# Optimization experiments

Measured on AMD Instinct MI355X. Metric: run time of the kernel, lower is better.

The kernel has to match this reference:

```python
import jax, jax.numpy as jnp
import numpy as np

NEG_SLOPE = 0.2  # PyG GATConv default negative_slope


def gat_layer(x, src, dst, W, a_src, a_dst, bias, concat, N):
    """PyG GATConv: h = xW; e_ij = LeakyReLU(a_src.h_j + a_dst.h_i);
    alpha = segment-softmax over incoming edges of i; out_i = sum_j alpha_ij h_j."""
    H, C = a_src.shape
    h = (x @ W).reshape(N, H, C)                      # [N,H,C]
    alpha_s = jnp.einsum('nhc,hc->nh', h, a_src)      # [N,H]
    alpha_d = jnp.einsum('nhc,hc->nh', h, a_dst)      # [N,H]
    e = jax.nn.leaky_relu(alpha_s[src] + alpha_d[dst], NEG_SLOPE)  # [E,H]
    # numerically-stable segment softmax over destination nodes
    m = jax.ops.segment_max(e, dst, num_segments=N)   # [N,H]
    e = jnp.exp(e - m[dst])
    denom = jax.ops.segment_sum(e, dst, num_segments=N)
    alpha = e / (denom[dst] + 1e-16)                  # [E,H]
    msg = h[src] * alpha[:, :, None]                  # [E,H,C]
    out = jax.ops.segment_sum(msg, dst, num_segments=N)  # [N,H,C]
    out = out.reshape(N, H * C) if concat else out.mean(axis=1)
    return out + bias


def setup_inputs() -> dict:
    key = jax.random.key(0)
    ks = jax.random.split(key, 12)
    N, E, F_IN, C, H = 50000, 800000, 512, 32, 8
    s = 0.05
    x = jax.random.normal(ks[0], (N, F_IN), dtype=jnp.float32)
    edge_index = jax.random.randint(ks[1], (2, E), 0, N, dtype=jnp.int64)
    W1 = jax.random.normal(ks[2], (F_IN, H * C), dtype=jnp.float32) * s
    as1 = jax.random.normal(ks[3], (H, C), dtype=jnp.float32) * s
    ad1 = jax.random.normal(ks[4], (H, C), dtype=jnp.float32) * s
    b1 = jnp.zeros((H * C,), dtype=jnp.float32)
    W2 = jax.random.normal(ks[5], (H * C, H * C), dtype=jnp.float32) * s
    as2 = jax.random.normal(ks[6], (H, C), dtype=jnp.float32) * s
    ad2 = jax.random.normal(ks[7], (H, C), dtype=jnp.float32) * s
    b2 = jnp.zeros((C,), dtype=jnp.float32)
    Wp = jax.random.normal(ks[8], (C, 1), dtype=jnp.float32) * s
    bp = jnp.zeros((1,), dtype=jnp.float32)
    return {"edge_index": edge_index, "x": x, "W1": W1, "as1": as1, "ad1": ad1,
            "b1": b1, "W2": W2, "as2": as2, "ad2": ad2, "b2": b2,
            "Wp": Wp, "bp": bp}


def reference(edge_index, x, W1, as1, ad1, b1, W2, as2, ad2, b2, Wp, bp):
    N = x.shape[0]
    # PyG GATConv adds self-loops by default
    loops = jnp.arange(N, dtype=edge_index.dtype)
    src = jnp.concatenate([edge_index[0], loops])
    dst = jnp.concatenate([edge_index[1], loops])
    h = gat_layer(x, src, dst, W1, as1, ad1, b1, concat=True, N=N)
    h = jax.nn.relu(h)
    # F.dropout(training=self.training) is identity in eval mode
    h = gat_layer(h, src, dst, W2, as2, ad2, b2, concat=False, N=N)
    return jax.nn.sigmoid(h @ Wp + bp)   # [N,1]
```

## Files before the change

### kernel.cpp

```cpp
#include <hip/hip_runtime.h>
#include <math.h>

#define H_HEADS 8
#define C_DIM   32
#define HC      256
#define F_IN    512
#define NEG_SLOPE 0.2f

typedef __attribute__((ext_vector_type(8))) short    bf16x8;
typedef __attribute__((ext_vector_type(4))) short    s16x4;
typedef __attribute__((ext_vector_type(4))) float    f32x4;
typedef __attribute__((ext_vector_type(2))) float    f32x2;
typedef __attribute__((ext_vector_type(8))) _Float16 h16x8;

__device__ __forceinline__ short f2bf(float f) {
    union { float f; unsigned u; } v; v.f = f;
    unsigned r = v.u + 0x7FFF + ((v.u >> 16) & 1);
    return (short)(r >> 16);
}

__device__ __forceinline__ void gl2lds16(const short* g, short* l) {
    __builtin_amdgcn_global_load_lds(
        (const __attribute__((address_space(1))) void*)g,
        (__attribute__((address_space(3))) void*)l, 16, 0, 0);
}

__global__ void wfrag_kernel(const float* __restrict__ W, short* __restrict__ Wf, int K)
{
    int tid = blockIdx.x * 256 + threadIdx.x;
    if (tid >= K * HC) return;
    int j  = tid & 7;
    int l  = (tid >> 3) & 63;
    int nb = (tid >> 9) & 15;
    int s  = tid >> 13;
    int k  = s * 32 + (l >> 4) * 8 + j;
    int n  = nb * 16 + (l & 15);
    Wf[tid] = f2bf(W[(size_t)k * HC + n]);
}

template<bool ABF16>
__global__ __launch_bounds__(256) void gemm_mfma(const void* __restrict__ Aptr,
    const short* __restrict__ Bf, unsigned char* __restrict__ h8,
    const float* __restrict__ a_s, const float* __restrict__ a_d,
    float* __restrict__ alpha_s, float* __restrict__ alpha_d, int M, int K)
{
    __shared__ short Bs[2][8192];
    __shared__ float Als[512], Ald[512];

    const int tid  = threadIdx.x;
    const int w    = tid >> 6;
    const int lane = tid & 63;
    const int quad = lane >> 4;
    const int ml   = lane & 15;
    const int bm   = blockIdx.x * 64;

    const int rowA = bm + w * 16 + ml;
    const int rowL = rowA < M ? rowA : M - 1;

    f32x4 acc[16];
    #pragma unroll
    for (int nb = 0; nb < 16; ++nb) acc[nb] = (f32x4){0.f, 0.f, 0.f, 0.f};

    const float* A32 = (const float*)Aptr;
    const short* A16 = (const short*)Aptr;
    const int nsteps = K >> 5;

    {
        const short* g = Bf + (size_t)w * 2048 + lane * 8;
        short* l = &Bs[0][w * 2048];
        #pragma unroll
        for (int c = 0; c < 4; ++c) gl2lds16(g + c * 512, l + c * 512);
    }

    float4 p0, p1;
    bf16x8 pb;
    if (ABF16) {
        pb = *(const bf16x8*)(A16 + (size_t)rowL * K + quad * 8);
    } else {
        const float* ap = A32 + (size_t)rowL * K + quad * 8;
        p0 = *(const float4*)(ap);
        p1 = *(const float4*)(ap + 4);
    }

    for (int s = 0; s < nsteps; ++s) {
        __syncthreads();

        if (s + 1 < nsteps) {
            const short* g = Bf + (size_t)(s + 1) * 8192 + w * 2048 + lane * 8;
            short* l = &Bs[(s + 1) & 1][w * 2048];
            #pragma unroll
            for (int c = 0; c < 4; ++c) gl2lds16(g + c * 512, l + c * 512);
        }

        bf16x8 af;
        if (ABF16) {
            af = pb;
            if (s + 1 < nsteps)
                pb = *(const bf16x8*)(A16 + (size_t)rowL * K + (s + 1) * 32 + quad * 8);
        } else {
            af[0] = f2bf(p0.x); af[1] = f2bf(p0.y); af[2] = f2bf(p0.z); af[3] = f2bf(p0.w);
            af[4] = f2bf(p1.x); af[5] = f2bf(p1.y); af[6] = f2bf(p1.z); af[7] = f2bf(p1.w);
            if (s + 1 < nsteps) {
                const float* ap = A32 + (size_t)rowL * K + (s + 1) * 32 + quad * 8;
                p0 = *(const float4*)(ap);
                p1 = *(const float4*)(ap + 4);
            }
        }

        const short* bsrc = &Bs[s & 1][lane * 8];
        #pragma unroll
        for (int nb = 0; nb < 16; ++nb) {
            bf16x8 bfr = *(const bf16x8*)(bsrc + nb * 512);
            acc[nb] = __builtin_amdgcn_mfma_f32_16x16x32_bf16(af, bfr, acc[nb], 0, 0, 0);
        }
    }

    float as_v[16], ad_v[16];
    #pragma unroll
    for (int nb = 0; nb < 16; ++nb) {
        as_v[nb] = a_s[nb * 16 + ml];
        ad_v[nb] = a_d[nb * 16 + ml];
    }

    #pragma unroll
    for (int r = 0; r < 4; ++r) {
        const int rl  = w * 16 + quad * 4 + r;
        const int row = bm + rl;

        if (row < M) {
            unsigned char* hrow = h8 + (size_t)row * HC;
            #pragma unroll
            for (int i = 0; i < 8; ++i) {
                int pk = __builtin_amdgcn_cvt_pk_fp8_f32(acc[2 * i][r], acc[2 * i + 1][r], 0, false);
                hrow[(2 * i) * 16 + ml]     = (unsigned char)(pk & 0xFF);
                hrow[(2 * i + 1) * 16 + ml] = (unsigned char)((pk >> 8) & 0xFF);
            }
        }

        float hs[8], hd[8];
        #pragma unroll
        for (int q = 0; q < 8; ++q) {
            hs[q] = acc[2 * q][r] * as_v[2 * q] + acc[2 * q + 1][r] * as_v[2 * q + 1];
            hd[q] = acc[2 * q][r] * ad_v[2 * q] + acc[2 * q + 1][r] * ad_v[2 * q + 1];
        }
        #pragma unroll
        for (int off = 1; off < 16; off <<= 1) {
            #pragma unroll
            for (int q = 0; q < 8; ++q) {
                hs[q] += __shfl_xor(hs[q], off);
                hd[q] += __shfl_xor(hd[q], off);
            }
        }
        if (ml == 0) {
            #pragma unroll
            for (int q = 0; q < 8; ++q) {
                Als[rl * 8 + q] = hs[q];
                Ald[rl * 8 + q] = hd[q];
            }
        }
    }
    __syncthreads();
    #pragma unroll
    for (int k = 0; k < 2; ++k) {
        int idx = tid + k * 256;
        int rl = idx >> 3, q = idx & 7;
        int row = bm + rl;
        if (row < M) {
            alpha_s[(size_t)row * H_HEADS + q] = Als[idx];
            alpha_d[(size_t)row * H_HEADS + q] = Ald[idx];
        }
    }
}

__global__ __launch_bounds__(256) void wcalc_kernel(const int2* __restrict__ es,
    const float* __restrict__ alpha_s, const float* __restrict__ alpha_d,
    _Float16* __restrict__ wq, int P)
{
    int p = blockIdx.x * 256 + threadIdx.x;
    if (p >= P) return;
    int2 sd = es[p];
    const float4* as = (const float4*)(alpha_s + (size_t)sd.x * H_HEADS);
    const float4* ad = (const float4*)(alpha_d + (size_t)sd.y * H_HEADS);
    float4 s0 = as[0], s1 = as[1], d0 = ad[0], d1 = ad[1];
    float e[8] = {s0.x + d0.x, s0.y + d0.y, s0.z + d0.z, s0.w + d0.w,
                  s1.x + d1.x, s1.y + d1.y, s1.z + d1.z, s1.w + d1.w};
    h16x8 o;
    #pragma unroll
    for (int h = 0; h < 8; ++h) {
        float v = e[h] > 0.f ? e[h] : NEG_SLOPE * e[h];
        o[h] = (_Float16)__expf(v);
    }
    *(h16x8*)(wq + (size_t)p * H_HEADS) = o;
}

__global__ void zero_int(int* __restrict__ p, int n)
{
    int i = blockIdx.x * 256 + threadIdx.x;
    if (i < n) p[i] = 0;
}

__global__ void hist_kernel(const int* __restrict__ ei, int E, int N,
                            int* __restrict__ cnt)
{
    int e = blockIdx.x * 256 + threadIdx.x;
    if (e < E) atomicAdd(&cnt[ei[E + e]], 1);
    else if (e < E + N) atomicAdd(&cnt[e - E], 1);
}

__global__ __launch_bounds__(256) void scan_sum(const int* __restrict__ cnt, int n,
                                                int* __restrict__ chunk_sum)
{
    __shared__ int lds[256];
    int b = blockIdx.x, t = threadIdx.x;
    int base = b * 1024 + t * 4;
    int s = 0;
    #pragma unroll
    for (int j = 0; j < 4; ++j) { int i = base + j; if (i < n) s += cnt[i]; }
    lds[t] = s; __syncthreads();
    for (int off = 128; off > 0; off >>= 1) {
        if (t < off) lds[t] += lds[t + off];
        __syncthreads();
    }
    if (t == 0) chunk_sum[b] = lds[0];
}

__global__ void scan_top(const int* __restrict__ chunk_sum, int nch,
                         int* __restrict__ chunk_off, int* __restrict__ row_ptr,
                         int n_nodes)
{
    int t = threadIdx.x;
    int v = (t < nch) ? chunk_sum[t] : 0;
    int inc = v;
    #pragma unroll
    for (int off = 1; off < 64; off <<= 1) {
        int u = __shfl_up(inc, off);
        if (t >= off) inc += u;
    }
    if (t < nch) chunk_off[t] = inc - v;
    if (t == 63) row_ptr[n_nodes] = inc;
}

__global__ __launch_bounds__(256) void scan_local(const int* __restrict__ cnt, int n,
    const int* __restrict__ chunk_off, int* __restrict__ row_ptr)
{
    __shared__ int lds[256];
    int b = blockIdx.x, t = threadIdx.x;
    int base = b * 1024 + t * 4;
    int v[4]; int s = 0;
    #pragma unroll
    for (int j = 0; j < 4; ++j) { int i = base + j; v[j] = (i < n) ? cnt[i] : 0; s += v[j]; }
    lds[t] = s; __syncthreads();
    for (int off = 1; off < 256; off <<= 1) {
        int u = (t >= off) ? lds[t - off] : 0;
        __syncthreads();
        lds[t] += u;
        __syncthreads();
    }
    int run = lds[t] - s + chunk_off[b];
    #pragma unroll
    for (int j = 0; j < 4; ++j) {
        int i = base + j;
        if (i < n) row_ptr[i] = run;
        run += v[j];
    }
}

__global__ void scatter_kernel(const int* __restrict__ ei, int E, int N,
    const int* __restrict__ row_ptr, int* __restrict__ fill, int2* __restrict__ es)
{
    int e = blockIdx.x * 256 + threadIdx.x;
    int src, dst;
    if (e < E)          { src = ei[e]; dst = ei[E + e]; }
    else if (e < E + N) { src = dst = e - E; }
    else return;
    int pos = row_ptr[dst] + atomicAdd(&fill[dst], 1);
    es[pos] = make_int2(src, dst);
}

__global__ __launch_bounds__(256) void agg1_kernel(const unsigned* __restrict__ h8,
    const _Float16* __restrict__ wq, const int* __restrict__ row_ptr,
    const int2* __restrict__ es, const float* __restrict__ bias,
    short* __restrict__ z_bf, int N)
{
    const int l = threadIdx.x & 63;
    const int i = blockIdx.x * 4 + (threadIdx.x >> 6);
    if (i >= N) return;
    const int hh = l >> 3;
    const int beg = row_ptr[i], end = row_ptr[i + 1];
    f32x4 acc = {0.f, 0.f, 0.f, 0.f};
    float dsum = 0.f;
    int p = beg;
    for (; p + 7 < end; p += 8) {
        int s[8]; float w[8]; unsigned hv[8];
        #pragma unroll
        for (int u = 0; u < 8; ++u) s[u] = es[p + u].x;
        #pragma unroll
        for (int u = 0; u < 8; ++u) w[u] = (float)wq[(size_t)(p + u) * 8 + hh];
        #pragma unroll
        for (int u = 0; u < 8; ++u) hv[u] = h8[(size_t)s[u] * 64 + l];
        #pragma unroll
        for (int u = 0; u < 8; ++u) {
            f32x2 lo = __builtin_amdgcn_cvt_pk_f32_fp8(hv[u], false);
            f32x2 hi = __builtin_amdgcn_cvt_pk_f32_fp8(hv[u], true);
            acc[0] = fmaf(w[u], lo[0], acc[0]);
            acc[1] = fmaf(w[u], lo[1], acc[1]);
            acc[2] = fmaf(w[u], hi[0], acc[2]);
            acc[3] = fmaf(w[u], hi[1], acc[3]);
            dsum += w[u];
        }
    }
    for (; p < end; ++p) {
        int s0 = es[p].x;
        float w0 = (float)wq[(size_t)p * 8 + hh];
        unsigned hv = h8[(size_t)s0 * 64 + l];
        f32x2 lo = __builtin_amdgcn_cvt_pk_f32_fp8(hv, false);
        f32x2 hi = __builtin_amdgcn_cvt_pk_f32_fp8(hv, true);
        acc[0] = fmaf(w0, lo[0], acc[0]);
        acc[1] = fmaf(w0, lo[1], acc[1]);
        acc[2] = fmaf(w0, hi[0], acc[2]);
        acc[3] = fmaf(w0, hi[1], acc[3]);
        dsum += w0;
    }
    float inv = 1.f / (dsum + 1e-16f);
    s16x4 pk;
    #pragma unroll
    for (int j = 0; j < 4; ++j) {
        float z = acc[j] * inv + bias[4 * l + j];
        pk[j] = f2bf(z > 0.f ? z : 0.f);
    }
    *(s16x4*)(z_bf + (size_t)i * HC + 4 * l) = pk;
}

__global__ __launch_bounds__(256) void agg2_kernel(const unsigned* __restrict__ h8,
    const _Float16* __restrict__ wq, const int* __restrict__ row_ptr,
    const int2* __restrict__ es, const float* __restrict__ b2,
    const float* __restrict__ Wp, const float* __restrict__ bp,
    float* __restrict__ out, int N)
{
    const int l = threadIdx.x & 63;
    const int i = blockIdx.x * 4 + (threadIdx.x >> 6);
    if (i >= N) return;
    const int hh = l >> 3;
    const int beg = row_ptr[i], end = row_ptr[i + 1];
    f32x4 acc = {0.f, 0.f, 0.f, 0.f};
    float dsum = 0.f;
    int p = beg;
    for (; p + 7 < end; p += 8) {
        int s[8]; float w[8]; unsigned hv[8];
        #pragma unroll
        for (int u = 0; u < 8; ++u) s[u] = es[p + u].x;
        #pragma unroll
        for (int u = 0; u < 8; ++u) w[u] = (float)wq[(size_t)(p + u) * 8 + hh];
        #pragma unroll
        for (int u = 0; u < 8; ++u) hv[u] = h8[(size_t)s[u] * 64 + l];
        #pragma unroll
        for (int u = 0; u < 8; ++u) {
            f32x2 lo = __builtin_amdgcn_cvt_pk_f32_fp8(hv[u], false);
            f32x2 hi = __builtin_amdgcn_cvt_pk_f32_fp8(hv[u], true);
            acc[0] = fmaf(w[u], lo[0], acc[0]);
            acc[1] = fmaf(w[u], lo[1], acc[1]);
            acc[2] = fmaf(w[u], hi[0], acc[2]);
            acc[3] = fmaf(w[u], hi[1], acc[3]);
            dsum += w[u];
        }
    }
    for (; p < end; ++p) {
        int s0 = es[p].x;
        float w0 = (float)wq[(size_t)p * 8 + hh];
        unsigned hv = h8[(size_t)s0 * 64 + l];
        f32x2 lo = __builtin_amdgcn_cvt_pk_f32_fp8(hv, false);
        f32x2 hi = __builtin_amdgcn_cvt_pk_f32_fp8(hv, true);
        acc[0] = fmaf(w0, lo[0], acc[0]);
        acc[1] = fmaf(w0, lo[1], acc[1]);
        acc[2] = fmaf(w0, hi[0], acc[2]);
        acc[3] = fmaf(w0, hi[1], acc[3]);
        dsum += w0;
    }
    float inv = 1.f / (dsum + 1e-16f);
    int cc = (4 * l) & 31;
    float partial = 0.f;
    #pragma unroll
    for (int j = 0; j < 4; ++j) partial = fmaf(acc[j] * inv, Wp[cc + j], partial);
    if (l < 8) {
        #pragma unroll
        for (int j = 0; j < 4; ++j) partial = fmaf(8.f * b2[4 * l + j], Wp[4 * l + j], partial);
    }
    #pragma unroll
    for (int off = 32; off > 0; off >>= 1) partial += __shfl_xor(partial, off);
    if (l == 0) out[i] = 1.f / (1.f + __expf(-(0.125f * partial + bp[0])));
}

extern "C" void kernel_launch(void* const* d_in, const int* in_sizes, int n_in,
                              void* d_out, int out_size, void* d_ws, size_t ws_size,
                              hipStream_t stream)
{
    const int*   ei  = (const int*)d_in[0];
    const float* x   = (const float*)d_in[1];
    const float* W1  = (const float*)d_in[2];
    const float* as1 = (const float*)d_in[3];
    const float* ad1 = (const float*)d_in[4];
    const float* b1  = (const float*)d_in[5];
    const float* W2  = (const float*)d_in[6];
    const float* as2 = (const float*)d_in[7];
    const float* ad2 = (const float*)d_in[8];
    const float* b2  = (const float*)d_in[9];
    const float* Wp  = (const float*)d_in[10];
    const float* bp  = (const float*)d_in[11];
    float* out = (float*)d_out;

    const int E = in_sizes[0] / 2;
    const int N = in_sizes[1] / F_IN;
    const int ET = E + N;

    float*         asb = (float*)d_ws;
    float*         adb = asb + (size_t)N * H_HEADS;
    unsigned char* h8  = (unsigned char*)(adb + (size_t)N * H_HEADS);
    short*         z1b = (short*)(h8 + (size_t)N * HC);
    short*         Wf1 = z1b + (size_t)N * HC;
    short*         Wf2 = Wf1 + (size_t)F_IN * HC;
    _Float16*      wq  = (_Float16*)(Wf2 + (size_t)HC * HC);
    int2*          es  = (int2*)(wq + (size_t)ET * H_HEADS);
    int* cnt       = (int*)(es + ET);
    int* fill      = cnt + N;
    int* row_ptr   = fill + N;
    int* chunk_off = row_ptr + N + 1;
    int* chunk_sum = chunk_off + 64;

    const int NCH = (N + 1023) / 1024;
    const int MB  = (N + 63) / 64;
    const int NB4 = (N + 3) / 4;

    zero_int<<<(2 * N + 255) / 256, 256, 0, stream>>>(cnt, 2 * N);
    hist_kernel<<<(ET + 255) / 256, 256, 0, stream>>>(ei, E, N, cnt);
    scan_sum<<<NCH, 256, 0, stream>>>(cnt, N, chunk_sum);
    scan_top<<<1, 64, 0, stream>>>(chunk_sum, NCH, chunk_off, row_ptr, N);
    scan_local<<<NCH, 256, 0, stream>>>(cnt, N, chunk_off, row_ptr);
    scatter_kernel<<<(ET + 255) / 256, 256, 0, stream>>>(ei, E, N, row_ptr, fill, es);

    wfrag_kernel<<<(F_IN * HC + 255) / 256, 256, 0, stream>>>(W1, Wf1, F_IN);
    wfrag_kernel<<<(HC * HC + 255) / 256, 256, 0, stream>>>(W2, Wf2, HC);

    gemm_mfma<false><<<MB, 256, 0, stream>>>(x, Wf1, h8, as1, ad1, asb, adb, N, F_IN);
    wcalc_kernel<<<(ET + 255) / 256, 256, 0, stream>>>(es, asb, adb, wq, ET);
    agg1_kernel<<<NB4, 256, 0, stream>>>((const unsigned*)h8, wq, row_ptr, es, b1, z1b, N);

    gemm_mfma<true><<<MB, 256, 0, stream>>>(z1b, Wf2, h8, as2, ad2, asb, adb, N, HC);
    wcalc_kernel<<<(ET + 255) / 256, 256, 0, stream>>>(es, asb, adb, wq, ET);
    agg2_kernel<<<NB4, 256, 0, stream>>>((const unsigned*)h8, wq, row_ptr, es, b2, Wp, bp, out, N);
}
```

Measured before the change: 423.2 us.

## Retile GEMM to 128-row blocks with 2x2 warp grid and packed bf16 convert

```diff
diff --git a/kernel.cpp b/kernel.cpp
--- a/kernel.cpp
+++ b/kernel.cpp
@@ -17,6 +17,15 @@
     union { float f; unsigned u; } v; v.f = f;
     unsigned r = v.u + 0x7FFF + ((v.u >> 16) & 1);
     return (short)(r >> 16);
+}
+
+__device__ __forceinline__ bf16x8 cvt8(float4 a, float4 b) {
+    union { bf16x8 v; unsigned u[4]; } r;
+    asm("v_cvt_pk_bf16_f32 %0, %1, %2" : "=v"(r.u[0]) : "v"(a.x), "v"(a.y));
+    asm("v_cvt_pk_bf16_f32 %0, %1, %2" : "=v"(r.u[1]) : "v"(a.z), "v"(a.w));
+    asm("v_cvt_pk_bf16_f32 %0, %1, %2" : "=v"(r.u[2]) : "v"(b.x), "v"(b.y));
+    asm("v_cvt_pk_bf16_f32 %0, %1, %2" : "=v"(r.u[3]) : "v"(b.z), "v"(b.w));
+    return r.v;
 }
 
 __device__ __forceinline__ void gl2lds16(const short* g, short* l) {
@@ -39,129 +48,177 @@
 }
 
 template<bool ABF16>
-__global__ __launch_bounds__(256) void gemm_mfma(const void* __restrict__ Aptr,
+__global__ __launch_bounds__(256, 2) void gemm_mfma(const void* __restrict__ Aptr,
     const short* __restrict__ Bf, unsigned char* __restrict__ h8,
     const float* __restrict__ a_s, const float* __restrict__ a_d,
     float* __restrict__ alpha_s, float* __restrict__ alpha_d, int M, int K)
 {
-    __shared__ short Bs[2][8192];
-    __shared__ float Als[512], Ald[512];
+    __shared__ short Bs[2][16384];
+    __shared__ float Als[1024], Ald[1024];
 
     const int tid  = threadIdx.x;
     const int w    = tid >> 6;
     const int lane = tid & 63;
     const int quad = lane >> 4;
     const int ml   = lane & 15;
-    const int bm   = blockIdx.x * 64;
-
-    const int rowA = bm + w * 16 + ml;
-    const int rowL = rowA < M ? rowA : M - 1;
-
-    f32x4 acc[16];
-    #pragma unroll
-    for (int nb = 0; nb < 16; ++nb) acc[nb] = (f32x4){0.f, 0.f, 0.f, 0.f};
+    const int wm   = w & 1;
+    const int wn   = w >> 1;
+    const int bm   = blockIdx.x * 128;
+
+    f32x4 acc[4][8];
+    #pragma unroll
+    for (int ff = 0; ff < 4; ++ff)
+        #pragma unroll
+        for (int nb = 0; nb < 8; ++nb) acc[ff][nb] = (f32x4){0.f, 0.f, 0.f, 0.f};
 
     const float* A32 = (const float*)Aptr;
     const short* A16 = (const short*)Aptr;
-    const int nsteps = K >> 5;
+    const int nph = K >> 6;
+
+    const float* ap32[4];
+    const short* ap16[4];
+    #pragma unroll
+    for (int ff = 0; ff < 4; ++ff) {
+        int row = bm + wm * 64 + ff * 16 + ml;
+        int rl  = row < M ? row : M - 1;
+        if (ABF16) ap16[ff] = A16 + (size_t)rl * K + quad * 8;
+        else       ap32[ff] = A32 + (size_t)rl * K + quad * 8;
+    }
 
     {
-        const short* g = Bf + (size_t)w * 2048 + lane * 8;
-        short* l = &Bs[0][w * 2048];
-        #pragma unroll
-        for (int c = 0; c < 4; ++c) gl2lds16(g + c * 512, l + c * 512);
-    }
-
-    float4 p0, p1;
-    bf16x8 pb;
+        const short* g = Bf + (size_t)w * 4096 + lane * 8;
+        short* l = &Bs[0][w * 4096];
+        #pragma unroll
+        for (int c = 0; c < 8; ++c) gl2lds16(g + c * 512, l + c * 512);
+    }
+
+    float4 pf[4][4];
+    bf16x8 pb[4][2];
     if (ABF16) {
-        pb = *(const bf16x8*)(A16 + (size_t)rowL * K + quad * 8);
+        #pragma unroll
+        for (int ff = 0; ff < 4; ++ff)
+            #pragma unroll
+            for (int kk = 0; kk < 2; ++kk)
+                pb[ff][kk] = *(const bf16x8*)(ap16[ff] + kk * 32);
     } else {
-        const float* ap = A32 + (size_t)rowL * K + quad * 8;
-        p0 = *(const float4*)(ap);
-        p1 = *(const float4*)(ap + 4);
-    }
-
-    for (int s = 0; s < nsteps; ++s) {
+        #pragma unroll
+        for (int ff = 0; ff < 4; ++ff)
+            #pragma unroll
+            for (int kk = 0; kk < 2; ++kk) {
+                pf[ff][2 * kk]     = *(const float4*)(ap32[ff] + kk * 32);
+                pf[ff][2 * kk + 1] = *(const float4*)(ap32[ff] + kk * 32 + 4);
+            }
+    }
+
+    for (int p = 0; p < nph; ++p) {
         __syncthreads();
 
-        if (s + 1 < nsteps) {
-            const short* g = Bf + (size_t)(s + 1) * 8192 + w * 2048 + lane * 8;
-            short* l = &Bs[(s + 1) & 1][w * 2048];
-            #pragma unroll
-            for (int c = 0; c < 4; ++c) gl2lds16(g + c * 512, l + c * 512);
-        }
-
-        bf16x8 af;
+        if (p + 1 < nph) {
+            const short* g = Bf + (size_t)(p + 1) * 16384 + w * 4096 + lane * 8;
+            short* l = &Bs[(p + 1) & 1][w * 4096];
+            #pragma unroll
+            for (int c = 0; c < 8; ++c) gl2lds16(g + c * 512, l + c * 512);
+        }
+
+        bf16x8 af[2][4];
         if (ABF16) {
-            af = pb;
-            if (s + 1 < nsteps)
-                pb = *(const bf16x8*)(A16 + (size_t)rowL * K + (s + 1) * 32 + quad * 8);
+            #pragma unroll
+            for (int kk = 0; kk < 2; ++kk)
+                #pragma unroll
+                for (int ff = 0; ff < 4; ++ff) af[kk][ff] = pb[ff][kk];
         } else {
-            af[0] = f2bf(p0.x); af[1] = f2bf(p0.y); af[2] = f2bf(p0.z); af[3] = f2bf(p0.w);
-            af[4] = f2bf(p1.x); af[5] = f2bf(p1.y); af[6] = f2bf(p1.z); af[7] = f2bf(p1.w);
-            if (s + 1 < nsteps) {
-                const float* ap = A32 + (size_t)rowL * K + (s + 1) * 32 + quad * 8;
-                p0 = *(const float4*)(ap);
-                p1 = *(const float4*)(ap + 4);
-            }
-        }
-
-        const short* bsrc = &Bs[s & 1][lane * 8];
-        #pragma unroll
-        for (int nb = 0; nb < 16; ++nb) {
-            bf16x8 bfr = *(const bf16x8*)(bsrc + nb * 512);
-            acc[nb] = __builtin_amdgcn_mfma_f32_16x16x32_bf16(af, bfr, acc[nb], 0, 0, 0);
-        }
-    }
-
-    float as_v[16], ad_v[16];
-    #pragma unroll
-    for (int nb = 0; nb < 16; ++nb) {
-        as_v[nb] = a_s[nb * 16 + ml];
-        ad_v[nb] = a_d[nb * 16 + ml];
-    }
-
-    #pragma unroll
-    for (int r = 0; r < 4; ++r) {
-        const int rl  = w * 16 + quad * 4 + r;
-        const int row = bm + rl;
-
-        if (row < M) {
-            unsigned char* hrow = h8 + (size_t)row * HC;
-            #pragma unroll
-            for (int i = 0; i < 8; ++i) {
-                int pk = __builtin_amdgcn_cvt_pk_fp8_f32(acc[2 * i][r], acc[2 * i + 1][r], 0, false);
-                hrow[(2 * i) * 16 + ml]     = (unsigned char)(pk & 0xFF);
-                hrow[(2 * i + 1) * 16 + ml] = (unsigned char)((pk >> 8) & 0xFF);
-            }
-        }
-
-        float hs[8], hd[8];
-        #pragma unroll
-        for (int q = 0; q < 8; ++q) {
-            hs[q] = acc[2 * q][r] * as_v[2 * q] + acc[2 * q + 1][r] * as_v[2 * q + 1];
-            hd[q] = acc[2 * q][r] * ad_v[2 * q] + acc[2 * q + 1][r] * ad_v[2 * q + 1];
-        }
-        #pragma unroll
-        for (int off = 1; off < 16; off <<= 1) {
-            #pragma unroll
-            for (int q = 0; q < 8; ++q) {
-                hs[q] += __shfl_xor(hs[q], off);
-                hd[q] += __shfl_xor(hd[q], off);
-            }
-        }
-        if (ml == 0) {
-            #pragma unroll
-            for (int q = 0; q < 8; ++q) {
-                Als[rl * 8 + q] = hs[q];
-                Ald[rl * 8 + q] = hd[q];
+            #pragma unroll
+            for (int kk = 0; kk < 2; ++kk)
+                #pragma unroll
+                for (int ff = 0; ff < 4; ++ff)
+                    af[kk][ff] = cvt8(pf[ff][2 * kk], pf[ff][2 * kk + 1]);
+        }
+
+        if (p + 1 < nph) {
+            const int kb = (p + 1) * 64;
+            if (ABF16) {
+                #pragma unroll
+                for (int ff = 0; ff < 4; ++ff)
+                    #pragma unroll
+                    for (int kk = 0; kk < 2; ++kk)
+                        pb[ff][kk] = *(const bf16x8*)(ap16[ff] + kb + kk * 32);
+            } else {
+                #pragma unroll
+                for (int ff = 0; ff < 4; ++ff)
+                    #pragma unroll
+                    for (int kk = 0; kk < 2; ++kk) {
+                        pf[ff][2 * kk]     = *(const float4*)(ap32[ff] + kb + kk * 32);
+                        pf[ff][2 * kk + 1] = *(const float4*)(ap32[ff] + kb + kk * 32 + 4);
+                    }
+            }
+        }
+
+        const short* bbase = &Bs[p & 1][(wn * 8) * 512 + lane * 8];
+        #pragma unroll
+        for (int kk = 0; kk < 2; ++kk) {
+            #pragma unroll
+            for (int nb = 0; nb < 8; ++nb) {
+                bf16x8 bfr = *(const bf16x8*)(bbase + kk * 8192 + nb * 512);
+                #pragma unroll
+                for (int ff = 0; ff < 4; ++ff)
+                    acc[ff][nb] = __builtin_amdgcn_mfma_f32_16x16x32_bf16(
+                        af[kk][ff], bfr, acc[ff][nb], 0, 0, 0);
+            }
+        }
+    }
+
+    float as_v[8], ad_v[8];
+    #pragma unroll
+    for (int nb = 0; nb < 8; ++nb) {
+        const int col = wn * 128 + nb * 16 + ml;
+        as_v[nb] = a_s[col];
+        ad_v[nb] = a_d[col];
+    }
+
+    #pragma unroll
+    for (int ff = 0; ff < 4; ++ff) {
+        #pragma unroll
+        for (int r = 0; r < 4; ++r) {
+            const int rl  = wm * 64 + ff * 16 + quad * 4 + r;
+            const int row = bm + rl;
+
+            if (row < M) {
+                unsigned char* hrow = h8 + (size_t)row * HC + wn * 128;
+                #pragma unroll
+                for (int i = 0; i < 4; ++i) {
+                    int pk = __builtin_amdgcn_cvt_pk_fp8_f32(
+                        acc[ff][2 * i][r], acc[ff][2 * i + 1][r], 0, false);
+                    hrow[(2 * i) * 16 + ml]     = (unsigned char)(pk & 0xFF);
+                    hrow[(2 * i + 1) * 16 + ml] = (unsigned char)((pk >> 8) & 0xFF);
+                }
+            }
+
+            float hs[4], hd[4];
+            #pragma unroll
+            for (int q = 0; q < 4; ++q) {
+                hs[q] = acc[ff][2 * q][r] * as_v[2 * q] + acc[ff][2 * q + 1][r] * as_v[2 * q + 1];
+                hd[q] = acc[ff][2 * q][r] * ad_v[2 * q] + acc[ff][2 * q + 1][r] * ad_v[2 * q + 1];
+            }
+            #pragma unroll
+            for (int off = 1; off < 16; off <<= 1) {
+                #pragma unroll
+                for (int q = 0; q < 4; ++q) {
+                    hs[q] += __shfl_xor(hs[q], off);
+                    hd[q] += __shfl_xor(hd[q], off);
+                }
+            }
+            if (ml == 0) {
+                #pragma unroll
+                for (int q = 0; q < 4; ++q) {
+                    Als[rl * 8 + wn * 4 + q] = hs[q];
+                    Ald[rl * 8 + wn * 4 + q] = hd[q];
+                }
             }
         }
     }
     __syncthreads();
     #pragma unroll
-    for (int k = 0; k < 2; ++k) {
+    for (int k = 0; k < 4; ++k) {
         int idx = tid + k * 256;
         int rl = idx >> 3, q = idx & 7;
         int row = bm + rl;
@@ -427,7 +484,7 @@
     int* chunk_sum = chunk_off + 64;
 
     const int NCH = (N + 1023) / 1024;
-    const int MB  = (N + 63) / 64;
+    const int MB  = (N + 127) / 128;
     const int NB4 = (N + 3) / 4;
 
     zero_int<<<(2 * N + 255) / 256, 256, 0, stream>>>(cnt, 2 * N);
```

New measurement: 421.7 us. About the same (-0.4%).

## Fuse edge-weight computation into aggregation and relax GEMM pipeline barriers

Applied to the files above, without the earlier changes.

```diff
diff --git a/kernel.cpp b/kernel.cpp
--- a/kernel.cpp
+++ b/kernel.cpp
@@ -11,12 +11,20 @@
 typedef __attribute__((ext_vector_type(4))) short    s16x4;
 typedef __attribute__((ext_vector_type(4))) float    f32x4;
 typedef __attribute__((ext_vector_type(2))) float    f32x2;
-typedef __attribute__((ext_vector_type(8))) _Float16 h16x8;
 
 __device__ __forceinline__ short f2bf(float f) {
     union { float f; unsigned u; } v; v.f = f;
     unsigned r = v.u + 0x7FFF + ((v.u >> 16) & 1);
     return (short)(r >> 16);
+}
+
+__device__ __forceinline__ bf16x8 cvt8(float4 a, float4 b) {
+    union { bf16x8 v; unsigned u[4]; } r;
+    asm("v_cvt_pk_bf16_f32 %0, %1, %2" : "=v"(r.u[0]) : "v"(a.x), "v"(a.y));
+    asm("v_cvt_pk_bf16_f32 %0, %1, %2" : "=v"(r.u[1]) : "v"(a.z), "v"(a.w));
+    asm("v_cvt_pk_bf16_f32 %0, %1, %2" : "=v"(r.u[2]) : "v"(b.x), "v"(b.y));
+    asm("v_cvt_pk_bf16_f32 %0, %1, %2" : "=v"(r.u[3]) : "v"(b.z), "v"(b.w));
+    return r.v;
 }
 
 __device__ __forceinline__ void gl2lds16(const short* g, short* l) {
@@ -71,6 +79,7 @@
         #pragma unroll
         for (int c = 0; c < 4; ++c) gl2lds16(g + c * 512, l + c * 512);
     }
+    __builtin_amdgcn_sched_barrier(0);
 
     float4 p0, p1;
     bf16x8 pb;
@@ -83,7 +92,9 @@
     }
 
     for (int s = 0; s < nsteps; ++s) {
-        __syncthreads();
+        if (ABF16) asm volatile("s_waitcnt vmcnt(1)" ::: "memory");
+        else       asm volatile("s_waitcnt vmcnt(2)" ::: "memory");
+        __builtin_amdgcn_s_barrier();
 
         if (s + 1 < nsteps) {
             const short* g = Bf + (size_t)(s + 1) * 8192 + w * 2048 + lane * 8;
@@ -91,6 +102,7 @@
             #pragma unroll
             for (int c = 0; c < 4; ++c) gl2lds16(g + c * 512, l + c * 512);
         }
+        __builtin_amdgcn_sched_barrier(0);
 
         bf16x8 af;
         if (ABF16) {
@@ -172,27 +184,6 @@
     }
 }
 
-__global__ __launch_bounds__(256) void wcalc_kernel(const int2* __restrict__ es,
-    const float* __restrict__ alpha_s, const float* __restrict__ alpha_d,
-    _Float16* __restrict__ wq, int P)
-{
-    int p = blockIdx.x * 256 + threadIdx.x;
-    if (p >= P) return;
-    int2 sd = es[p];
-    const float4* as = (const float4*)(alpha_s + (size_t)sd.x * H_HEADS);
-    const float4* ad = (const float4*)(alpha_d + (size_t)sd.y * H_HEADS);
-    float4 s0 = as[0], s1 = as[1], d0 = ad[0], d1 = ad[1];
-    float e[8] = {s0.x + d0.x, s0.y + d0.y, s0.z + d0.z, s0.w + d0.w,
-                  s1.x + d1.x, s1.y + d1.y, s1.z + d1.z, s1.w + d1.w};
-    h16x8 o;
-    #pragma unroll
-    for (int h = 0; h < 8; ++h) {
-        float v = e[h] > 0.f ? e[h] : NEG_SLOPE * e[h];
-        o[h] = (_Float16)__expf(v);
-    }
-    *(h16x8*)(wq + (size_t)p * H_HEADS) = o;
-}
-
 __global__ void zero_int(int* __restrict__ p, int n)
 {
     int i = blockIdx.x * 256 + threadIdx.x;
@@ -266,7 +257,7 @@
 }
 
 __global__ void scatter_kernel(const int* __restrict__ ei, int E, int N,
-    const int* __restrict__ row_ptr, int* __restrict__ fill, int2* __restrict__ es)
+    const int* __restrict__ row_ptr, int* __restrict__ fill, int* __restrict__ es)
 {
     int e = blockIdx.x * 256 + threadIdx.x;
     int src, dst;
@@ -274,44 +265,48 @@
     else if (e < E + N) { src = dst = e - E; }
     else return;
     int pos = row_ptr[dst] + atomicAdd(&fill[dst], 1);
-    es[pos] = make_int2(src, dst);
+    es[pos] = src;
 }
 
 __global__ __launch_bounds__(256) void agg1_kernel(const unsigned* __restrict__ h8,
-    const _Float16* __restrict__ wq, const int* __restrict__ row_ptr,
-    const int2* __restrict__ es, const float* __restrict__ bias,
-    short* __restrict__ z_bf, int N)
+    const float* __restrict__ asb, const float* __restrict__ adb,
+    const int* __restrict__ row_ptr, const int* __restrict__ es,
+    const float* __restrict__ bias, short* __restrict__ z_bf, int N)
 {
     const int l = threadIdx.x & 63;
     const int i = blockIdx.x * 4 + (threadIdx.x >> 6);
     if (i >= N) return;
     const int hh = l >> 3;
+    const float ad8 = adb[(size_t)i * 8 + hh];
     const int beg = row_ptr[i], end = row_ptr[i + 1];
     f32x4 acc = {0.f, 0.f, 0.f, 0.f};
     float dsum = 0.f;
     int p = beg;
     for (; p + 7 < end; p += 8) {
-        int s[8]; float w[8]; unsigned hv[8];
-        #pragma unroll
-        for (int u = 0; u < 8; ++u) s[u] = es[p + u].x;
-        #pragma unroll
-        for (int u = 0; u < 8; ++u) w[u] = (float)wq[(size_t)(p + u) * 8 + hh];
+        int s[8]; float av[8]; unsigned hv[8];
+        #pragma unroll
+        for (int u = 0; u < 8; ++u) s[u] = es[p + u];
+        #pragma unroll
+        for (int u = 0; u < 8; ++u) av[u] = asb[(size_t)s[u] * 8 + hh];
         #pragma unroll
         for (int u = 0; u < 8; ++u) hv[u] = h8[(size_t)s[u] * 64 + l];
         #pragma unroll
         for (int u = 0; u < 8; ++u) {
+            float e = av[u] + ad8;
+            float w = __expf(e > 0.f ? e : NEG_SLOPE * e);
             f32x2 lo = __builtin_amdgcn_cvt_pk_f32_fp8(hv[u], false);
             f32x2 hi = __builtin_amdgcn_cvt_pk_f32_fp8(hv[u], true);
-            acc[0] = fmaf(w[u], lo[0], acc[0]);
-            acc[1] = fmaf(w[u], lo[1], acc[1]);
-            acc[2] = fmaf(w[u], hi[0], acc[2]);
-            acc[3] = fmaf(w[u], hi[1], acc[3]);
-            dsum += w[u];
+            acc[0] = fmaf(w, lo[0], acc[0]);
+            acc[1] = fmaf(w, lo[1], acc[1]);
+            acc[2] = fmaf(w, hi[0], acc[2]);
+            acc[3] = fmaf(w, hi[1], acc[3]);
+            dsum += w;
         }
     }
     for (; p < end; ++p) {
-        int s0 = es[p].x;
-        float w0 = (float)wq[(size_t)p * 8 + hh];
+        int s0 = es[p];
+        float e = asb[(size_t)s0 * 8 + hh] + ad8;
+        float w0 = __expf(e > 0.f ? e : NEG_SLOPE * e);
         unsigned hv = h8[(size_t)s0 * 64 + l];
         f32x2 lo = __builtin_amdgcn_cvt_pk_f32_fp8(hv, false);
         f32x2 hi = __builtin_amdgcn_cvt_pk_f32_fp8(hv, true);
@@ -332,41 +327,45 @@
 }
 
 __global__ __launch_bounds__(256) void agg2_kernel(const unsigned* __restrict__ h8,
-    const _Float16* __restrict__ wq, const int* __restrict__ row_ptr,
-    const int2* __restrict__ es, const float* __restrict__ b2,
-    const float* __restrict__ Wp, const float* __restrict__ bp,
-    float* __restrict__ out, int N)
+    const float* __restrict__ asb, const float* __restrict__ adb,
+    const int* __restrict__ row_ptr, const int* __restrict__ es,
+    const float* __restrict__ b2, const float* __restrict__ Wp,
+    const float* __restrict__ bp, float* __restrict__ out, int N)
 {
     const int l = threadIdx.x & 63;
     const int i = blockIdx.x * 4 + (threadIdx.x >> 6);
     if (i >= N) return;
     const int hh = l >> 3;
+    const float ad8 = adb[(size_t)i * 8 + hh];
     const int beg = row_ptr[i], end = row_ptr[i + 1];
     f32x4 acc = {0.f, 0.f, 0.f, 0.f};
     float dsum = 0.f;
     int p = beg;
     for (; p + 7 < end; p += 8) {
-        int s[8]; float w[8]; unsigned hv[8];
-        #pragma unroll
-        for (int u = 0; u < 8; ++u) s[u] = es[p + u].x;
-        #pragma unroll
-        for (int u = 0; u < 8; ++u) w[u] = (float)wq[(size_t)(p + u) * 8 + hh];
+        int s[8]; float av[8]; unsigned hv[8];
+        #pragma unroll
+        for (int u = 0; u < 8; ++u) s[u] = es[p + u];
+        #pragma unroll
+        for (int u = 0; u < 8; ++u) av[u] = asb[(size_t)s[u] * 8 + hh];
         #pragma unroll
         for (int u = 0; u < 8; ++u) hv[u] = h8[(size_t)s[u] * 64 + l];
         #pragma unroll
         for (int u = 0; u < 8; ++u) {
+            float e = av[u] + ad8;
+            float w = __expf(e > 0.f ? e : NEG_SLOPE * e);
             f32x2 lo = __builtin_amdgcn_cvt_pk_f32_fp8(hv[u], false);
             f32x2 hi = __builtin_amdgcn_cvt_pk_f32_fp8(hv[u], true);
-            acc[0] = fmaf(w[u], lo[0], acc[0]);
-            acc[1] = fmaf(w[u], lo[1], acc[1]);
-            acc[2] = fmaf(w[u], hi[0], acc[2]);
-            acc[3] = fmaf(w[u], hi[1], acc[3]);
-            dsum += w[u];
+            acc[0] = fmaf(w, lo[0], acc[0]);
+            acc[1] = fmaf(w, lo[1], acc[1]);
+            acc[2] = fmaf(w, hi[0], acc[2]);
+            acc[3] = fmaf(w, hi[1], acc[3]);
+            dsum += w;
         }
     }
     for (; p < end; ++p) {
-        int s0 = es[p].x;
-        float w0 = (float)wq[(size_t)p * 8 + hh];
+        int s0 = es[p];
+        float e = asb[(size_t)s0 * 8 + hh] + ad8;
+        float w0 = __expf(e > 0.f ? e : NEG_SLOPE * e);
         unsigned hv = h8[(size_t)s0 * 64 + l];
         f32x2 lo = __builtin_amdgcn_cvt_pk_f32_fp8(hv, false);
         f32x2 hi = __builtin_amdgcn_cvt_pk_f32_fp8(hv, true);
@@ -418,9 +417,8 @@
     short*         z1b = (short*)(h8 + (size_t)N * HC);
     short*         Wf1 = z1b + (size_t)N * HC;
     short*         Wf2 = Wf1 + (size_t)F_IN * HC;
-    _Float16*      wq  = (_Float16*)(Wf2 + (size_t)HC * HC);
-    int2*          es  = (int2*)(wq + (size_t)ET * H_HEADS);
-    int* cnt       = (int*)(es + ET);
+    int*           es  = (int*)(Wf2 + (size_t)HC * HC);
+    int* cnt       = es + ET;
     int* fill      = cnt + N;
     int* row_ptr   = fill + N;
     int* chunk_off = row_ptr + N + 1;
@@ -441,10 +439,8 @@
     wfrag_kernel<<<(HC * HC + 255) / 256, 256, 0, stream>>>(W2, Wf2, HC);
 
     gemm_mfma<false><<<MB, 256, 0, stream>>>(x, Wf1, h8, as1, ad1, asb, adb, N, F_IN);
-    wcalc_kernel<<<(ET + 255) / 256, 256, 0, stream>>>(es, asb, adb, wq, ET);
-    agg1_kernel<<<NB4, 256, 0, stream>>>((const unsigned*)h8, wq, row_ptr, es, b1, z1b, N);
+    agg1_kernel<<<NB4, 256, 0, stream>>>((const unsigned*)h8, asb, adb, row_ptr, es, b1, z1b, N);
 
     gemm_mfma<true><<<MB, 256, 0, stream>>>(z1b, Wf2, h8, as2, ad2, asb, adb, N, HC);
-    wcalc_kernel<<<(ET + 255) / 256, 256, 0, stream>>>(es, asb, adb, wq, ET);
-    agg2_kernel<<<NB4, 256, 0, stream>>>((const unsigned*)h8, wq, row_ptr, es, b2, Wp, bp, out, N);
-}
+    agg2_kernel<<<NB4, 256, 0, stream>>>((const unsigned*)h8, asb, adb, row_ptr, es, b2, Wp, bp, out, N);
+}
```

Measured after the change: 436.2 us. 3.1% more time.

## Pre-convert x to bf16 in fused prep kernel and reuse count buffer for scatter

Applied to the files above, without the earlier changes.

```diff
diff --git a/kernel.cpp b/kernel.cpp
--- a/kernel.cpp
+++ b/kernel.cpp
@@ -19,27 +19,57 @@
     return (short)(r >> 16);
 }
 
+__device__ __forceinline__ bf16x8 cvt8(float4 a, float4 b) {
+    union { bf16x8 v; unsigned u[4]; } r;
+    asm("v_cvt_pk_bf16_f32 %0, %1, %2" : "=v"(r.u[0]) : "v"(a.x), "v"(a.y));
+    asm("v_cvt_pk_bf16_f32 %0, %1, %2" : "=v"(r.u[1]) : "v"(a.z), "v"(a.w));
+    asm("v_cvt_pk_bf16_f32 %0, %1, %2" : "=v"(r.u[2]) : "v"(b.x), "v"(b.y));
+    asm("v_cvt_pk_bf16_f32 %0, %1, %2" : "=v"(r.u[3]) : "v"(b.z), "v"(b.w));
+    return r.v;
+}
+
 __device__ __forceinline__ void gl2lds16(const short* g, short* l) {
     __builtin_amdgcn_global_load_lds(
         (const __attribute__((address_space(1))) void*)g,
         (__attribute__((address_space(3))) void*)l, 16, 0, 0);
 }
 
-__global__ void wfrag_kernel(const float* __restrict__ W, short* __restrict__ Wf, int K)
-{
+__global__ __launch_bounds__(256) void prep_kernel(const float* __restrict__ W1,
+    const float* __restrict__ W2, const float* __restrict__ x,
+    short* __restrict__ Wf1, short* __restrict__ Wf2, short* __restrict__ xbf,
+    int nx)
+{
+    const int NW1 = F_IN * HC;
+    const int NW2 = HC * HC;
     int tid = blockIdx.x * 256 + threadIdx.x;
-    if (tid >= K * HC) return;
-    int j  = tid & 7;
-    int l  = (tid >> 3) & 63;
-    int nb = (tid >> 9) & 15;
-    int s  = tid >> 13;
-    int k  = s * 32 + (l >> 4) * 8 + j;
-    int n  = nb * 16 + (l & 15);
-    Wf[tid] = f2bf(W[(size_t)k * HC + n]);
-}
-
-template<bool ABF16>
-__global__ __launch_bounds__(256) void gemm_mfma(const void* __restrict__ Aptr,
+    if (tid < NW1) {
+        int j  = tid & 7;
+        int l  = (tid >> 3) & 63;
+        int nb = (tid >> 9) & 15;
+        int s  = tid >> 13;
+        int k  = s * 32 + (l >> 4) * 8 + j;
+        int n  = nb * 16 + (l & 15);
+        Wf1[tid] = f2bf(W1[(size_t)k * HC + n]);
+    } else if (tid < NW1 + NW2) {
+        int t  = tid - NW1;
+        int j  = t & 7;
+        int l  = (t >> 3) & 63;
+        int nb = (t >> 9) & 15;
+        int s  = t >> 13;
+        int k  = s * 32 + (l >> 4) * 8 + j;
+        int n  = nb * 16 + (l & 15);
+        Wf2[t] = f2bf(W2[(size_t)k * HC + n]);
+    } else {
+        size_t idx = (size_t)(tid - NW1 - NW2) * 8;
+        if (idx < (size_t)nx) {
+            float4 a = *(const float4*)(x + idx);
+            float4 b = *(const float4*)(x + idx + 4);
+            *(bf16x8*)(xbf + idx) = cvt8(a, b);
+        }
+    }
+}
+
+__global__ __launch_bounds__(256) void gemm_mfma(const short* __restrict__ A16,
     const short* __restrict__ Bf, unsigned char* __restrict__ h8,
     const float* __restrict__ a_s, const float* __restrict__ a_d,
     float* __restrict__ alpha_s, float* __restrict__ alpha_d, int M, int K)
@@ -61,8 +91,6 @@
     #pragma unroll
     for (int nb = 0; nb < 16; ++nb) acc[nb] = (f32x4){0.f, 0.f, 0.f, 0.f};
 
-    const float* A32 = (const float*)Aptr;
-    const short* A16 = (const short*)Aptr;
     const int nsteps = K >> 5;
 
     {
@@ -72,15 +100,7 @@
         for (int c = 0; c < 4; ++c) gl2lds16(g + c * 512, l + c * 512);
     }
 
-    float4 p0, p1;
-    bf16x8 pb;
-    if (ABF16) {
-        pb = *(const bf16x8*)(A16 + (size_t)rowL * K + quad * 8);
-    } else {
-        const float* ap = A32 + (size_t)rowL * K + quad * 8;
-        p0 = *(const float4*)(ap);
-        p1 = *(const float4*)(ap + 4);
-    }
+    bf16x8 pb = *(const bf16x8*)(A16 + (size_t)rowL * K + quad * 8);
 
     for (int s = 0; s < nsteps; ++s) {
         __syncthreads();
@@ -92,20 +112,9 @@
             for (int c = 0; c < 4; ++c) gl2lds16(g + c * 512, l + c * 512);
         }
 
-        bf16x8 af;
-        if (ABF16) {
-            af = pb;
-            if (s + 1 < nsteps)
-                pb = *(const bf16x8*)(A16 + (size_t)rowL * K + (s + 1) * 32 + quad * 8);
-        } else {
-            af[0] = f2bf(p0.x); af[1] = f2bf(p0.y); af[2] = f2bf(p0.z); af[3] = f2bf(p0.w);
-            af[4] = f2bf(p1.x); af[5] = f2bf(p1.y); af[6] = f2bf(p1.z); af[7] = f2bf(p1.w);
-            if (s + 1 < nsteps) {
-                const float* ap = A32 + (size_t)rowL * K + (s + 1) * 32 + quad * 8;
-                p0 = *(const float4*)(ap);
-                p1 = *(const float4*)(ap + 4);
-            }
-        }
+        bf16x8 af = pb;
+        if (s + 1 < nsteps)
+            pb = *(const bf16x8*)(A16 + (size_t)rowL * K + (s + 1) * 32 + quad * 8);
 
         const short* bsrc = &Bs[s & 1][lane * 8];
         #pragma unroll
@@ -266,14 +275,14 @@
 }
 
 __global__ void scatter_kernel(const int* __restrict__ ei, int E, int N,
-    const int* __restrict__ row_ptr, int* __restrict__ fill, int2* __restrict__ es)
+    const int* __restrict__ row_ptr, int* __restrict__ cnt, int2* __restrict__ es)
 {
     int e = blockIdx.x * 256 + threadIdx.x;
     int src, dst;
     if (e < E)          { src = ei[e]; dst = ei[E + e]; }
     else if (e < E + N) { src = dst = e - E; }
     else return;
-    int pos = row_ptr[dst] + atomicAdd(&fill[dst], 1);
+    int pos = row_ptr[dst] + atomicSub(&cnt[dst], 1) - 1;
     es[pos] = make_int2(src, dst);
 }
 
@@ -415,36 +424,37 @@
     float*         asb = (float*)d_ws;
     float*         adb = asb + (size_t)N * H_HEADS;
     unsigned char* h8  = (unsigned char*)(adb + (size_t)N * H_HEADS);
-    short*         z1b = (short*)(h8 + (size_t)N * HC);
-    short*         Wf1 = z1b + (size_t)N * HC;
+    short*         xz  = (short*)(h8 + (size_t)N * HC);
+    short*         xbf = xz;
+    short*         z1b = xz;
+    short*         Wf1 = xz + (size_t)N * F_IN;
     short*         Wf2 = Wf1 + (size_t)F_IN * HC;
     _Float16*      wq  = (_Float16*)(Wf2 + (size_t)HC * HC);
     int2*          es  = (int2*)(wq + (size_t)ET * H_HEADS);
     int* cnt       = (int*)(es + ET);
-    int* fill      = cnt + N;
-    int* row_ptr   = fill + N;
+    int* row_ptr   = cnt + N;
     int* chunk_off = row_ptr + N + 1;
     int* chunk_sum = chunk_off + 64;
 
     const int NCH = (N + 1023) / 1024;
     const int MB  = (N + 63) / 64;
     const int NB4 = (N + 3) / 4;
-
-    zero_int<<<(2 * N + 255) / 256, 256, 0, stream>>>(cnt, 2 * N);
+    const int NPREP = (F_IN * HC + HC * HC + (N * F_IN) / 8 + 255) / 256;
+
+    zero_int<<<(N + 255) / 256, 256, 0, stream>>>(cnt, N);
     hist_kernel<<<(ET + 255) / 256, 256, 0, stream>>>(ei, E, N, cnt);
     scan_sum<<<NCH, 256, 0, stream>>>(cnt, N, chunk_sum);
     scan_top<<<1, 64, 0, stream>>>(chunk_sum, NCH, chunk_off, row_ptr, N);
     scan_local<<<NCH, 256, 0, stream>>>(cnt, N, chunk_off, row_ptr);
-    scatter_kernel<<<(ET + 255) / 256, 256, 0, stream>>>(ei, E, N, row_ptr, fill, es);
-
-    wfrag_kernel<<<(F_IN * HC + 255) / 256, 256, 0, stream>>>(W1, Wf1, F_IN);
-    wfrag_kernel<<<(HC * HC + 255) / 256, 256, 0, stream>>>(W2, Wf2, HC);
-
-    gemm_mfma<false><<<MB, 256, 0, stream>>>(x, Wf1, h8, as1, ad1, asb, adb, N, F_IN);
+    scatter_kernel<<<(ET + 255) / 256, 256, 0, stream>>>(ei, E, N, row_ptr, cnt, es);
+
+    prep_kernel<<<NPREP, 256, 0, stream>>>(W1, W2, x, Wf1, Wf2, xbf, N * F_IN);
+
+    gemm_mfma<<<MB, 256, 0, stream>>>(xbf, Wf1, h8, as1, ad1, asb, adb, N, F_IN);
     wcalc_kernel<<<(ET + 255) / 256, 256, 0, stream>>>(es, asb, adb, wq, ET);
     agg1_kernel<<<NB4, 256, 0, stream>>>((const unsigned*)h8, wq, row_ptr, es, b1, z1b, N);
 
-    gemm_mfma<true><<<MB, 256, 0, stream>>>(z1b, Wf2, h8, as2, ad2, asb, adb, N, HC);
+    gemm_mfma<<<MB, 256, 0, stream>>>(z1b, Wf2, h8, as2, ad2, asb, adb, N, HC);
     wcalc_kernel<<<(ET + 255) / 256, 256, 0, stream>>>(es, asb, adb, wq, ET);
     agg2_kernel<<<NB4, 256, 0, stream>>>((const unsigned*)h8, wq, row_ptr, es, b2, Wp, bp, out, N);
 }
```

New measurement: 445.1 us. 1.05x slower.
